# Kernel optimization log

Measured on AMD Instinct MI355X. Metric: run time of the kernel, lower is better.

## Reference

```python
import jax, jax.numpy as jnp
import numpy as np

# init_kwargs baked as constants
GAMMA = 0.1
QTSE_WEIGHT = 1.0
SOFT_DTW_WEIGHT = 0.1
KQTSE = 0.1
BIG = 1e10  # finite stand-in for +inf so gradients stay NaN-free


def setup_inputs() -> dict:
    key = jax.random.key(0)
    k1, k2 = jax.random.split(key)
    predicted = jax.random.normal(k1, (32, 1024), dtype=jnp.float32)
    target = jax.random.normal(k2, (32, 1024), dtype=jnp.float32)
    return {"predicted": predicted, "target": target}


def _softmin3(a, b, c, gamma):
    # -gamma * log(exp(-a/g) + exp(-b/g) + exp(-c/g)), numerically stable
    z = jnp.stack([a, b, c]) * (-1.0 / gamma)
    return -gamma * jax.nn.logsumexp(z, axis=0)


def _soft_dtw(D, gamma):
    """Soft-DTW value per batch element.
    D: [B, N, M] pairwise squared distances. Returns [B].
    R[0,0]=0, R[i,0]=R[0,j]=inf; R[i,j] = D[i,j] + softmin(R[i-1,j-1], R[i-1,j], R[i,j-1]).
    Row-wise lax.scan (outer over i) with an inner scan over j carrying R[i,j-1].
    """
    B, N, M = D.shape
    big = jnp.asarray(BIG, D.dtype)
    # R[0, 0:M+1] = [0, inf, ..., inf]
    r0 = jnp.concatenate([jnp.zeros((B, 1), D.dtype),
                          jnp.full((B, M), big, D.dtype)], axis=1)  # [B, M+1]

    def row_step(r_prev, d_row):  # r_prev: [B, M+1] = R[i-1, :]; d_row: [M, B]
        r_diag = jnp.transpose(r_prev[:, :-1])  # [M, B] -> R[i-1, j-1]
        r_up = jnp.transpose(r_prev[:, 1:])     # [M, B] -> R[i-1, j]

        def col_step(r_left, inp):
            d, rd, ru = inp  # each [B]
            r = d + _softmin3(rd, ru, r_left, gamma)
            return r, r

        _, row = jax.lax.scan(col_step, jnp.full((B,), big, D.dtype),
                              (d_row, r_diag, r_up))  # row: [M, B] = R[i, 1:]
        r_new = jnp.concatenate([jnp.full((B, 1), big, D.dtype),
                                 jnp.transpose(row)], axis=1)  # [B, M+1]
        return r_new, None

    # xs over rows i=1..N: D rearranged to [N, M, B]
    r_final, _ = jax.lax.scan(row_step, r0, jnp.transpose(D, (1, 2, 0)))
    return r_final[:, -1]  # R[N, M] per batch element


def reference(predicted, target):
    # QTSE: quadratic loss with exponential asymmetry
    error = predicted - target
    qtse = jnp.mean(error ** 2 * jnp.exp(KQTSE * error))
    # soft-DTW between 1-d sequences: D[b,i,j] = (p_i - t_j)^2
    D = (predicted[:, :, None] - target[:, None, :]) ** 2  # [B, T, T]
    sdtw = jnp.mean(_soft_dtw(D, GAMMA))
    return SOFT_DTW_WEIGHT * sdtw + QTSE_WEIGHT * qtse
```

## Files before the change

kernel.cpp:

```cpp
#include <hip/hip_runtime.h>
#include <hip/hip_bf16.h>

#define BATCH 32
#define T 1024
#define WVS 8
#define NTH (WVS * 64)
#define KS 8
#define DOW 71
#define BIGF 1e10f
#define K2f 14.426950408889634f
#define GLN2f 0.0693147180559945f
#define KQTSE_ 0.1f

#define DG (BATCH * T)
#define OFF_AF 0
#define OFF_BF DG
#define OFF_AB (2 * DG)
#define OFF_BB (3 * DG)
#define SDTW_OFFF (4 * DG)
#define WS_NEEDED ((size_t)(4 * DG + 2 * BATCH) * 4)

__device__ __forceinline__ float fexp2(float x) {
    float r;
    asm("v_exp_f32 %0, %1" : "=v"(r) : "v"(x));
    return r;
}

__device__ __forceinline__ float softmin3(float a, float b, float c) {
    float m  = fminf(fminf(a, b), c);
    float M  = fmaxf(fmaxf(a, b), c);
    float md = __builtin_amdgcn_fmed3f(a, b, c);
    float mk = m * K2f;
    float e1 = fexp2(fmaf(-K2f, md, mk));
    float e2 = fexp2(fmaf(-K2f, M, mk));
    return fmaf(-GLN2f, __log2f(1.0f + e1 + e2), m);
}

__device__ __forceinline__ float lane_shr1(float old, float src) {
    return __int_as_float(__builtin_amdgcn_update_dpp(
        __float_as_int(old), __float_as_int(src), 0x138, 0xF, 0xF, false));
}

__global__ __launch_bounds__(NTH) void sdtw_half(const float* __restrict__ pred,
                                                 const float* __restrict__ targ,
                                                 float* __restrict__ ws) {
    __shared__ float p[T];
    __shared__ float ring[WVS - 1][T];

    const int blk = blockIdx.x;
    const int b = blk & (BATCH - 1);
    const int dir = blk >> 5;
    const int tid = threadIdx.x;
    const int wv = tid >> 6;
    const int ln = tid & 63;
    const int rank = (wv < 4) ? (2 * wv) : (15 - 2 * wv);
    const int vtid = (rank << 6) + ln;
    const int myoff = DOW * rank + ln;

    const float2 pv2 = ((const float2*)(pred + b * T))[tid];
    if (dir == 0) {
        ((float2*)p)[tid] = pv2;
    } else {
        p[T - 1 - 2 * tid] = pv2.x;
        p[T - 2 - 2 * tid] = pv2.y;
    }
    const int c0g = dir ? (T - 1 - 2 * vtid) : (2 * vtid);
    const int c1g = dir ? (T - 2 - 2 * vtid) : (2 * vtid + 1);
    const float tj0 = targ[b * T + c0g];
    const float tj1 = targ[b * T + c1g];
    const float zcc = (vtid == 0) ? 0.0f : BIGF;

    const int q = (dir ? 1023 : 1021) - 2 * vtid;
    const int nb = 128 + dir;
    const int wA = (DOW * rank) >> 3;
    const int wB = (1022 + 2 * dir - 57 * rank) >> 3;

    float top0 = BIGF, top1 = BIGF, corner = BIGF, rc = BIGF;
    float rA0 = BIGF, rB0 = BIGF, rA1 = BIGF, rB1 = BIGF;

    __syncthreads();

    for (int sb = 0; sb < nb; ++sb) {
        if (sb >= wA && sb <= wB) {
            const int ics = sb * KS - myoff;

            float rl[KS];
#pragma unroll
            for (int so = 0; so < KS; ++so) rl[so] = BIGF;
            if (ln == 0 && rank > 0) {
#pragma unroll
                for (int so = 0; so < KS; ++so) rl[so] = ring[rank - 1][(ics + so) & (T - 1)];
            }

            float Dv0[KS], Dv1[KS];
#pragma unroll
            for (int so = 0; so < KS; ++so) {
                const float pr = p[(ics + so) & (T - 1)];
                const float d0 = pr - tj0;
                const float d1 = pr - tj1;
                Dv0[so] = d0 * d0;
                Dv1[so] = d1 * d1;
            }

#pragma unroll
            for (int so = 0; so < KS; ++so) {
                const int ic = ics + so;
                const float lf = lane_shr1(rl[so], rc);
                const bool r0 = (ic == 0);
                const float t0 = r0 ? BIGF : top0;
                const float t1 = r0 ? BIGF : top1;
                const float cc = r0 ? zcc : corner;

                const float c00 = Dv0[so] + softmin3(cc, t0, lf);
                const float c01 = Dv1[so] + softmin3(t0, t1, c00);

                if (ic == q - 1) rA1 = c01;
                if (ic == q)     { rA0 = c00; rB1 = c01; }
                if (ic == q + 1) rB0 = c00;

                rc = c01; top0 = c00; top1 = c01; corner = lf;
                if (ln == 63 && rank < WVS - 1 && (unsigned)ic < (unsigned)T)
                    ring[rank][ic] = c01;
            }
        }
        __syncthreads();
    }

    float* dgA = ws + (dir ? OFF_AB : OFF_AF) + b * T;
    float* dgB = ws + (dir ? OFF_BB : OFF_BF) + b * T;
    dgA[2 * vtid] = rA0;
    dgA[2 * vtid + 1] = rA1;
    dgB[2 * vtid] = rB0;
    dgB[2 * vtid + 1] = rB1;
}

__global__ __launch_bounds__(1024) void merge_kernel(const float* __restrict__ pred,
                                                     const float* __restrict__ targ,
                                                     float* __restrict__ ws) {
    const int b = blockIdx.x;
    const int tid = threadIdx.x;
    const float* dgAf = ws + OFF_AF + b * T;
    const float* dgBf = ws + OFF_BF + b * T;
    const float* dgAb = ws + OFF_AB + b * T;
    const float* dgBb = ws + OFF_BB + b * T;

    float t1 = BIGF, t2 = BIGF;
    if (tid >= 1) {
        const float d = pred[b * T + tid - 1] - targ[b * T + 1023 - tid];
        t1 = dgBf[1023 - tid] + dgBb[tid] - d * d;
    }
    if (tid >= 1 && tid <= 1022) {
        t2 = dgAf[1022 - tid] + dgAb[tid];
    }
    const float e = pred[b * T + tid] - targ[b * T + tid];
    float qacc = e * e * __expf(KQTSE_ * e);

    __shared__ float red[16];
    __shared__ float redq[16];
    __shared__ float bcast;
    const int wv = tid >> 6, ln = tid & 63;

    float mn = fminf(t1, t2);
    for (int off = 32; off; off >>= 1) mn = fminf(mn, __shfl_xor(mn, off, 64));
    if (ln == 0) red[wv] = mn;
    __syncthreads();
    if (tid == 0) {
        float m = red[0];
        for (int w = 1; w < 16; ++w) m = fminf(m, red[w]);
        bcast = m;
    }
    __syncthreads();
    const float m = bcast;

    float s = fexp2((m - t1) * K2f) + fexp2((m - t2) * K2f);
    for (int off = 32; off; off >>= 1) s += __shfl_xor(s, off, 64);
    for (int off = 32; off; off >>= 1) qacc += __shfl_xor(qacc, off, 64);
    __syncthreads();
    if (ln == 0) { red[wv] = s; redq[wv] = qacc; }
    __syncthreads();
    if (tid == 0) {
        float tot = 0.0f, qt = 0.0f;
        for (int w = 0; w < 16; ++w) { tot += red[w]; qt += redq[w]; }
        ws[SDTW_OFFF + b] = fmaf(-GLN2f, __log2f(tot), m);
        ws[SDTW_OFFF + BATCH + b] = qt;
    }
}

__global__ __launch_bounds__(64) void finish_small(const float* __restrict__ sd,
                                                   float* __restrict__ out) {
    const int l = threadIdx.x;
    float s = (l < BATCH) ? sd[l] : 0.0f;
    float qv = (l < BATCH) ? sd[BATCH + l] : 0.0f;
    for (int off = 32; off; off >>= 1) {
        s += __shfl_down(s, off, 64);
        qv += __shfl_down(qv, off, 64);
    }
    if (l == 0) out[0] = 0.1f * (s / (float)BATCH) + qv / (float)(BATCH * T);
}

#define FB_KS 16
#define FB_DOW 79
#define FB_NB 83

__global__ __launch_bounds__(256) void sdtw_fb(const float* __restrict__ pred,
                                               const float* __restrict__ targ,
                                               float* __restrict__ sdtw_out) {
    __shared__ float p[T];
    __shared__ float ring[3][T];
    const int b = blockIdx.x;
    const int tid = threadIdx.x;
    const int wv = tid >> 6, ln = tid & 63;
    const int myoff = FB_DOW * wv + ln;
    ((float4*)p)[tid] = ((const float4*)(pred + b * T))[tid];
    const float4 t4 = ((const float4*)(targ + b * T))[tid];
    const float tj0 = t4.x, tj1 = t4.y, tj2 = t4.z, tj3 = t4.w;
    const float zcc = (tid == 0) ? 0.0f : BIGF;
    float top0 = BIGF, top1 = BIGF, top2 = BIGF, top3 = BIGF;
    float corner = BIGF, rc = BIGF, result = 0.0f;
    __syncthreads();
    for (int sb = 0; sb < FB_NB; ++sb) {
        const int ics = sb * FB_KS - myoff;
        float rl[FB_KS];
#pragma unroll
        for (int so = 0; so < FB_KS; ++so) rl[so] = BIGF;
        if (ln == 0 && wv > 0) {
#pragma unroll
            for (int so = 0; so < FB_KS; ++so) rl[so] = ring[wv - 1][(ics + so) & (T - 1)];
        }
        float Dv0[FB_KS], Dv1[FB_KS], Dv2[FB_KS], Dv3[FB_KS];
#pragma unroll
        for (int so = 0; so < FB_KS; ++so) {
            const float pr = p[(ics + so) & (T - 1)];
            const float d0 = pr - tj0, d1 = pr - tj1, d2 = pr - tj2, d3 = pr - tj3;
            Dv0[so] = d0 * d0; Dv1[so] = d1 * d1; Dv2[so] = d2 * d2; Dv3[so] = d3 * d3;
        }
#pragma unroll
        for (int so = 0; so < FB_KS; ++so) {
            const int ic = ics + so;
            const float lf = lane_shr1(rl[so], rc);
            const bool r0 = (ic == 0);
            const float t0 = r0 ? BIGF : top0;
            const float t1 = r0 ? BIGF : top1;
            const float t2 = r0 ? BIGF : top2;
            const float t3 = r0 ? BIGF : top3;
            const float cc = r0 ? zcc : corner;
            const float c0 = Dv0[so] + softmin3(cc, t0, lf);
            const float c1 = Dv1[so] + softmin3(t0, t1, c0);
            const float c2 = Dv2[so] + softmin3(t1, t2, c1);
            const float c3 = Dv3[so] + softmin3(t2, t3, c2);
            rc = c3; top0 = c0; top1 = c1; top2 = c2; top3 = c3;
            corner = lf;
            if ((unsigned)ic < (unsigned)T) result = c3;
            if (ln == 63 && wv < 3 && (unsigned)ic < (unsigned)T) ring[wv][ic] = c3;
        }
        __syncthreads();
    }
    if (tid == 255) sdtw_out[b] = result;
}

__global__ __launch_bounds__(1024) void finish_kernel(const float* __restrict__ pred,
                                                      const float* __restrict__ targ,
                                                      const float* __restrict__ sdtw,
                                                      float* __restrict__ out) {
    const int tid = threadIdx.x;
    float acc = 0.0f;
    for (int idx = tid; idx < BATCH * T; idx += 1024) {
        const float e = pred[idx] - targ[idx];
        acc += e * e * __expf(KQTSE_ * e);
    }
    for (int off = 32; off; off >>= 1) acc += __shfl_down(acc, off, 64);
    __shared__ float red[16];
    const int wave = tid >> 6, lane = tid & 63;
    if (lane == 0) red[wave] = acc;
    __syncthreads();
    if (tid == 0) {
        float qv = 0.0f;
        for (int w = 0; w < 16; ++w) qv += red[w];
        qv /= (float)(BATCH * T);
        float s = 0.0f;
        for (int bb = 0; bb < BATCH; ++bb) s += sdtw[bb];
        s /= (float)BATCH;
        out[0] = 0.1f * s + 1.0f * qv;
    }
}

extern "C" void kernel_launch(void* const* d_in, const int* in_sizes, int n_in,
                              void* d_out, int out_size, void* d_ws, size_t ws_size,
                              hipStream_t stream) {
    const float* pred = (const float*)d_in[0];
    const float* targ = (const float*)d_in[1];
    float* out = (float*)d_out;

    if (ws_size >= WS_NEEDED) {
        float* ws = (float*)d_ws;
        sdtw_half<<<BATCH * 2, NTH, 0, stream>>>(pred, targ, ws);
        merge_kernel<<<BATCH, 1024, 0, stream>>>(pred, targ, ws);
        finish_small<<<1, 64, 0, stream>>>(ws + SDTW_OFFF, out);
    } else {
        float* sdtw = (float*)d_ws;
        sdtw_fb<<<BATCH, 256, 0, stream>>>(pred, targ, sdtw);
        finish_kernel<<<1, 1024, 0, stream>>>(pred, targ, sdtw, out);
    }
}
```

Before: 172.6 us.

## Split each soft-DTW half into two column panels linked by a global-memory spin handoff

```diff
diff --git a/kernel.cpp b/kernel.cpp
--- a/kernel.cpp
+++ b/kernel.cpp
@@ -4,7 +4,7 @@
 #define BATCH 32
 #define T 1024
 #define WVS 8
-#define NTH (WVS * 64)
+#define NTH 512
 #define KS 8
 #define DOW 71
 #define BIGF 1e10f
@@ -18,7 +18,13 @@
 #define OFF_AB (2 * DG)
 #define OFF_BB (3 * DG)
 #define SDTW_OFFF (4 * DG)
-#define WS_NEEDED ((size_t)(4 * DG + 2 * BATCH) * 4)
+#define EDGE_OFF (4 * DG + 2 * BATCH)
+#define EDGE_FLTS 544
+#define WS1 ((size_t)(4 * DG + 2 * BATCH) * 4)
+#define WS2 ((size_t)(EDGE_OFF + 64 * EDGE_FLTS) * 4)
+#define SENT_U 0xAAAAAAAAu
+
+typedef float f32x4 __attribute__((ext_vector_type(4)));
 
 __device__ __forceinline__ float fexp2(float x) {
     float r;
@@ -41,12 +47,171 @@
         __float_as_int(old), __float_as_int(src), 0x138, 0xF, 0xF, false));
 }
 
-__global__ __launch_bounds__(NTH) void sdtw_half(const float* __restrict__ pred,
-                                                 const float* __restrict__ targ,
-                                                 float* __restrict__ ws) {
+__device__ __forceinline__ void issue_load8(const float* base, f32x4& a, f32x4& b) {
+    asm volatile("global_load_dwordx4 %0, %2, off sc0 sc1\n\t"
+                 "global_load_dwordx4 %1, %2, off offset:16 sc0 sc1"
+                 : "=&v"(a), "=&v"(b) : "v"(base));
+}
+__device__ __forceinline__ void await_load8(f32x4& a, f32x4& b) {
+    asm volatile("s_waitcnt vmcnt(0)" : "+v"(a), "+v"(b) :: "memory");
+    __builtin_amdgcn_sched_barrier(0);
+}
+__device__ __forceinline__ bool has_sent(const f32x4& a, const f32x4& b) {
+    return (__float_as_uint(a.x) == SENT_U) | (__float_as_uint(a.y) == SENT_U) |
+           (__float_as_uint(a.z) == SENT_U) | (__float_as_uint(a.w) == SENT_U) |
+           (__float_as_uint(b.x) == SENT_U) | (__float_as_uint(b.y) == SENT_U) |
+           (__float_as_uint(b.z) == SENT_U) | (__float_as_uint(b.w) == SENT_U);
+}
+__device__ __forceinline__ void spin_load8(const float* base, f32x4& a, f32x4& b) {
+    issue_load8(base, a, b);
+    await_load8(a, b);
+    while (has_sent(a, b)) {
+        __builtin_amdgcn_s_sleep(8);
+        issue_load8(base, a, b);
+        await_load8(a, b);
+    }
+}
+__device__ __forceinline__ void store_edge8(float* base, const f32x4& a, const f32x4& b) {
+    asm volatile("global_store_dwordx4 %0, %1, off sc0 sc1\n\t"
+                 "global_store_dwordx4 %0, %2, off offset:16 sc0 sc1"
+                 :: "v"(base), "v"(a), "v"(b) : "memory");
+}
+
+__global__ __launch_bounds__(NTH) void sdtw_panel(const float* __restrict__ pred,
+                                                  const float* __restrict__ targ,
+                                                  float* __restrict__ ws) {
     __shared__ float p[T];
     __shared__ float ring[WVS - 1][T];
 
+    const int blk = blockIdx.x;
+    const int b = blk & (BATCH - 1);
+    const int dir = (blk >> 5) & 1;
+    const int pg = blk >> 6;
+    const int tid = threadIdx.x;
+    const int wv = tid >> 6;
+    const int ln = tid & 63;
+    const int rank = (wv < 4) ? (2 * wv) : (15 - 2 * wv);
+    const int vtid = (rank << 6) + ln;
+    const int j = pg * 512 + vtid;
+    const int myoff = DOW * rank + ln;
+
+    const float2 pv2 = ((const float2*)(pred + b * T))[tid];
+    if (dir == 0) {
+        ((float2*)p)[tid] = pv2;
+    } else {
+        p[T - 1 - 2 * tid] = pv2.x;
+        p[T - 2 - 2 * tid] = pv2.y;
+    }
+    const float tj = targ[b * T + (dir ? (T - 1 - j) : j)];
+    const float zcc = (j == 0) ? 0.0f : BIGF;
+
+    const int q = (dir ? 1023 : 1021) - j;
+    const int qp1 = q + 1;
+    const int wA = myoff >> 3;
+    const int wB = (1022 + 2 * dir - pg * 512 + 7 * rank) >> 3;
+    const int nbl = ((1022 + 2 * dir - pg * 512 + 49) >> 3) + 1;
+    const int nch = ((510 + 2 * dir) >> 3) + 1;
+
+    float* eb = ws + EDGE_OFF + (b + BATCH * dir) * EDGE_FLTS;
+    const bool consumer = (pg == 1) && (tid == 0);
+    const bool producing = (pg == 0) && (rank == 7) && (ln == 63);
+
+    float top = BIGF, corner = BIGF, rc = BIGF;
+    float rA = BIGF, rB = BIGF;
+    float rlg[KS];
+#pragma unroll
+    for (int i = 0; i < KS; ++i) rlg[i] = BIGF;
+
+    __syncthreads();
+
+    if (consumer) {
+        f32x4 a, b4;
+        spin_load8(eb + 3 * KS, a, b4);
+        spin_load8(eb, a, b4);
+        rlg[0] = a.x; rlg[1] = a.y; rlg[2] = a.z; rlg[3] = a.w;
+        rlg[4] = b4.x; rlg[5] = b4.y; rlg[6] = b4.z; rlg[7] = b4.w;
+    }
+
+    for (int sb = 0; sb < nbl; ++sb) {
+        if (sb >= wA && sb <= wB) {
+            const int ics = sb * KS - myoff;
+
+            float rl[KS];
+#pragma unroll
+            for (int so = 0; so < KS; ++so) rl[so] = BIGF;
+            if (ln == 0) {
+                if (rank > 0) {
+#pragma unroll
+                    for (int so = 0; so < KS; ++so) rl[so] = ring[rank - 1][(ics + so) & (T - 1)];
+                } else if (pg == 1) {
+#pragma unroll
+                    for (int so = 0; so < KS; ++so) rl[so] = rlg[so];
+                }
+            }
+
+            float Dv[KS];
+#pragma unroll
+            for (int so = 0; so < KS; ++so) {
+                const float d = p[(ics + so) & (T - 1)] - tj;
+                Dv[so] = d * d;
+            }
+
+            f32x4 na, nb4;
+            const bool want = consumer && (sb + 1) < nch;
+            const float* basep = eb + (sb + 1) * KS;
+            if (want) issue_load8(basep, na, nb4);
+
+            float erow[KS];
+#pragma unroll
+            for (int so = 0; so < KS; ++so) {
+                const int ic = ics + so;
+                const float lf = lane_shr1(rl[so], rc);
+                const bool r0 = (ic == 0);
+                const float t0 = r0 ? BIGF : top;
+                const float cc = r0 ? zcc : corner;
+
+                const float c00 = Dv[so] + softmin3(cc, t0, lf);
+
+                if (ic == q)   rA = c00;
+                if (ic == qp1) rB = c00;
+
+                rc = c00; top = c00; corner = lf;
+                erow[so] = (ic <= qp1) ? c00 : 0.0f;
+                if (ln == 63 && rank < WVS - 1 && (unsigned)ic < (unsigned)T)
+                    ring[rank][ic] = c00;
+            }
+
+            if (producing && ics >= 0) {
+                f32x4 ea = {erow[0], erow[1], erow[2], erow[3]};
+                f32x4 eb2 = {erow[4], erow[5], erow[6], erow[7]};
+                store_edge8(eb + ics, ea, eb2);
+            }
+
+            if (want) {
+                await_load8(na, nb4);
+                while (has_sent(na, nb4)) {
+                    __builtin_amdgcn_s_sleep(2);
+                    issue_load8(basep, na, nb4);
+                    await_load8(na, nb4);
+                }
+                rlg[0] = na.x; rlg[1] = na.y; rlg[2] = na.z; rlg[3] = na.w;
+                rlg[4] = nb4.x; rlg[5] = nb4.y; rlg[6] = nb4.z; rlg[7] = nb4.w;
+            }
+        }
+        __syncthreads();
+    }
+
+    float* dgA = ws + (dir ? OFF_AB : OFF_AF) + b * T;
+    float* dgB = ws + (dir ? OFF_BB : OFF_BF) + b * T;
+    dgA[j] = rA;
+    dgB[j] = rB;
+}
+
+__global__ __launch_bounds__(NTH) void sdtw_half_g(const float* __restrict__ pred,
+                                                   const float* __restrict__ targ,
+                                                   float* __restrict__ ws) {
+    __shared__ float p[T];
+    __shared__ float ring[WVS - 1][T];
     const int blk = blockIdx.x;
     const int b = blk & (BATCH - 1);
     const int dir = blk >> 5;
@@ -56,7 +221,6 @@
     const int rank = (wv < 4) ? (2 * wv) : (15 - 2 * wv);
     const int vtid = (rank << 6) + ln;
     const int myoff = DOW * rank + ln;
-
     const float2 pv2 = ((const float2*)(pred + b * T))[tid];
     if (dir == 0) {
         ((float2*)p)[tid] = pv2;
@@ -69,21 +233,16 @@
     const float tj0 = targ[b * T + c0g];
     const float tj1 = targ[b * T + c1g];
     const float zcc = (vtid == 0) ? 0.0f : BIGF;
-
     const int q = (dir ? 1023 : 1021) - 2 * vtid;
     const int nb = 128 + dir;
     const int wA = (DOW * rank) >> 3;
     const int wB = (1022 + 2 * dir - 57 * rank) >> 3;
-
     float top0 = BIGF, top1 = BIGF, corner = BIGF, rc = BIGF;
     float rA0 = BIGF, rB0 = BIGF, rA1 = BIGF, rB1 = BIGF;
-
-    __syncthreads();
-
+    __syncthreads();
     for (int sb = 0; sb < nb; ++sb) {
         if (sb >= wA && sb <= wB) {
             const int ics = sb * KS - myoff;
-
             float rl[KS];
 #pragma unroll
             for (int so = 0; so < KS; ++so) rl[so] = BIGF;
@@ -91,7 +250,6 @@
 #pragma unroll
                 for (int so = 0; so < KS; ++so) rl[so] = ring[rank - 1][(ics + so) & (T - 1)];
             }
-
             float Dv0[KS], Dv1[KS];
 #pragma unroll
             for (int so = 0; so < KS; ++so) {
@@ -101,7 +259,6 @@
                 Dv0[so] = d0 * d0;
                 Dv1[so] = d1 * d1;
             }
-
 #pragma unroll
             for (int so = 0; so < KS; ++so) {
                 const int ic = ics + so;
@@ -110,14 +267,11 @@
                 const float t0 = r0 ? BIGF : top0;
                 const float t1 = r0 ? BIGF : top1;
                 const float cc = r0 ? zcc : corner;
-
                 const float c00 = Dv0[so] + softmin3(cc, t0, lf);
                 const float c01 = Dv1[so] + softmin3(t0, t1, c00);
-
                 if (ic == q - 1) rA1 = c01;
                 if (ic == q)     { rA0 = c00; rB1 = c01; }
                 if (ic == q + 1) rB0 = c00;
-
                 rc = c01; top0 = c00; top1 = c01; corner = lf;
                 if (ln == 63 && rank < WVS - 1 && (unsigned)ic < (unsigned)T)
                     ring[rank][ic] = c01;
@@ -125,7 +279,6 @@
         }
         __syncthreads();
     }
-
     float* dgA = ws + (dir ? OFF_AB : OFF_AF) + b * T;
     float* dgB = ws + (dir ? OFF_BB : OFF_BF) + b * T;
     dgA[2 * vtid] = rA0;
@@ -198,107 +351,20 @@
     if (l == 0) out[0] = 0.1f * (s / (float)BATCH) + qv / (float)(BATCH * T);
 }
 
-#define FB_KS 16
-#define FB_DOW 79
-#define FB_NB 83
-
-__global__ __launch_bounds__(256) void sdtw_fb(const float* __restrict__ pred,
-                                               const float* __restrict__ targ,
-                                               float* __restrict__ sdtw_out) {
-    __shared__ float p[T];
-    __shared__ float ring[3][T];
-    const int b = blockIdx.x;
-    const int tid = threadIdx.x;
-    const int wv = tid >> 6, ln = tid & 63;
-    const int myoff = FB_DOW * wv + ln;
-    ((float4*)p)[tid] = ((const float4*)(pred + b * T))[tid];
-    const float4 t4 = ((const float4*)(targ + b * T))[tid];
-    const float tj0 = t4.x, tj1 = t4.y, tj2 = t4.z, tj3 = t4.w;
-    const float zcc = (tid == 0) ? 0.0f : BIGF;
-    float top0 = BIGF, top1 = BIGF, top2 = BIGF, top3 = BIGF;
-    float corner = BIGF, rc = BIGF, result = 0.0f;
-    __syncthreads();
-    for (int sb = 0; sb < FB_NB; ++sb) {
-        const int ics = sb * FB_KS - myoff;
-        float rl[FB_KS];
-#pragma unroll
-        for (int so = 0; so < FB_KS; ++so) rl[so] = BIGF;
-        if (ln == 0 && wv > 0) {
-#pragma unroll
-            for (int so = 0; so < FB_KS; ++so) rl[so] = ring[wv - 1][(ics + so) & (T - 1)];
-        }
-        float Dv0[FB_KS], Dv1[FB_KS], Dv2[FB_KS], Dv3[FB_KS];
-#pragma unroll
-        for (int so = 0; so < FB_KS; ++so) {
-            const float pr = p[(ics + so) & (T - 1)];
-            const float d0 = pr - tj0, d1 = pr - tj1, d2 = pr - tj2, d3 = pr - tj3;
-            Dv0[so] = d0 * d0; Dv1[so] = d1 * d1; Dv2[so] = d2 * d2; Dv3[so] = d3 * d3;
-        }
-#pragma unroll
-        for (int so = 0; so < FB_KS; ++so) {
-            const int ic = ics + so;
-            const float lf = lane_shr1(rl[so], rc);
-            const bool r0 = (ic == 0);
-            const float t0 = r0 ? BIGF : top0;
-            const float t1 = r0 ? BIGF : top1;
-            const float t2 = r0 ? BIGF : top2;
-            const float t3 = r0 ? BIGF : top3;
-            const float cc = r0 ? zcc : corner;
-            const float c0 = Dv0[so] + softmin3(cc, t0, lf);
-            const float c1 = Dv1[so] + softmin3(t0, t1, c0);
-            const float c2 = Dv2[so] + softmin3(t1, t2, c1);
-            const float c3 = Dv3[so] + softmin3(t2, t3, c2);
-            rc = c3; top0 = c0; top1 = c1; top2 = c2; top3 = c3;
-            corner = lf;
-            if ((unsigned)ic < (unsigned)T) result = c3;
-            if (ln == 63 && wv < 3 && (unsigned)ic < (unsigned)T) ring[wv][ic] = c3;
-        }
-        __syncthreads();
-    }
-    if (tid == 255) sdtw_out[b] = result;
-}
-
-__global__ __launch_bounds__(1024) void finish_kernel(const float* __restrict__ pred,
-                                                      const float* __restrict__ targ,
-                                                      const float* __restrict__ sdtw,
-                                                      float* __restrict__ out) {
-    const int tid = threadIdx.x;
-    float acc = 0.0f;
-    for (int idx = tid; idx < BATCH * T; idx += 1024) {
-        const float e = pred[idx] - targ[idx];
-        acc += e * e * __expf(KQTSE_ * e);
-    }
-    for (int off = 32; off; off >>= 1) acc += __shfl_down(acc, off, 64);
-    __shared__ float red[16];
-    const int wave = tid >> 6, lane = tid & 63;
-    if (lane == 0) red[wave] = acc;
-    __syncthreads();
-    if (tid == 0) {
-        float qv = 0.0f;
-        for (int w = 0; w < 16; ++w) qv += red[w];
-        qv /= (float)(BATCH * T);
-        float s = 0.0f;
-        for (int bb = 0; bb < BATCH; ++bb) s += sdtw[bb];
-        s /= (float)BATCH;
-        out[0] = 0.1f * s + 1.0f * qv;
-    }
-}
-
 extern "C" void kernel_launch(void* const* d_in, const int* in_sizes, int n_in,
                               void* d_out, int out_size, void* d_ws, size_t ws_size,
                               hipStream_t stream) {
     const float* pred = (const float*)d_in[0];
     const float* targ = (const float*)d_in[1];
     float* out = (float*)d_out;
-
-    if (ws_size >= WS_NEEDED) {
-        float* ws = (float*)d_ws;
-        sdtw_half<<<BATCH * 2, NTH, 0, stream>>>(pred, targ, ws);
-        merge_kernel<<<BATCH, 1024, 0, stream>>>(pred, targ, ws);
-        finish_small<<<1, 64, 0, stream>>>(ws + SDTW_OFFF, out);
+    float* ws = (float*)d_ws;
+
+    if (ws_size >= WS2) {
+        hipMemsetAsync((char*)d_ws + EDGE_OFF * 4, 0xAA, 64 * EDGE_FLTS * 4, stream);
+        sdtw_panel<<<BATCH * 4, NTH, 0, stream>>>(pred, targ, ws);
     } else {
-        float* sdtw = (float*)d_ws;
-        sdtw_fb<<<BATCH, 256, 0, stream>>>(pred, targ, sdtw);
-        finish_kernel<<<1, 1024, 0, stream>>>(pred, targ, sdtw, out);
-    }
-}
+        sdtw_half_g<<<BATCH * 2, NTH, 0, stream>>>(pred, targ, ws);
+    }
+    merge_kernel<<<BATCH, 1024, 0, stream>>>(pred, targ, ws);
+    finish_small<<<1, 64, 0, stream>>>(ws + SDTW_OFFF, out);
+}
```

Result: no change. 171.6 us, median of 2 (-0.6%).
